# Kernel tuning notes

Measured on AMD Instinct MI355X. Metric: run time of the kernel, lower is better.

## Reference

```python
import jax, jax.numpy as jnp
import numpy as np

N = 20000          # nodes
E = 320000         # directed edges (self-loops added in reference)
F_IN = 128         # input node features
HEADS = 8
HID = 64           # per-head hidden channels
G = 64             # graphs in the batch
NUM_CLASSES = 10
NEG_SLOPE = 0.2    # PyG GATConv LeakyReLU slope


def _gat_layer(x, src, dst, W, a_src, a_dst, bias, n_nodes):
    """PyG-style GATConv: messages flow src->dst, softmax over incoming edges."""
    H, C = a_src.shape
    h = (x @ W).reshape(n_nodes, H, C)                     # [N,H,C]
    asrc = jnp.einsum('nhc,hc->nh', h, a_src)              # [N,H]
    adst = jnp.einsum('nhc,hc->nh', h, a_dst)              # [N,H]
    e = jax.nn.leaky_relu(asrc[src] + adst[dst], NEG_SLOPE)  # [Etot,H]
    emax = jax.ops.segment_max(e, dst, num_segments=n_nodes)  # [N,H]
    ee = jnp.exp(e - emax[dst])
    denom = jax.ops.segment_sum(ee, dst, num_segments=n_nodes)
    alpha = ee / (denom[dst] + 1e-16)                      # [Etot,H]
    out = jax.ops.segment_sum(h[src] * alpha[:, :, None], dst, num_segments=n_nodes)
    return out.reshape(n_nodes, H * C) + bias


def setup_inputs() -> dict:
    key = jax.random.key(0)
    ks = jax.random.split(key, 10)
    x = jax.random.normal(ks[0], (N, F_IN), jnp.float32)
    edge_index = jax.random.randint(ks[1], (2, E), 0, N, jnp.int32)
    batch = jnp.sort(jax.random.randint(ks[2], (N,), 0, G, jnp.int32))
    # layer 1: F_IN -> HEADS*HID (concat)
    W1 = jax.random.normal(ks[3], (F_IN, HEADS * HID), jnp.float32) / np.float32(np.sqrt(F_IN))
    a_src1 = jax.random.normal(ks[4], (HEADS, HID), jnp.float32) / np.float32(np.sqrt(HID))
    a_dst1 = jax.random.normal(ks[5], (HEADS, HID), jnp.float32) / np.float32(np.sqrt(HID))
    b1 = jnp.zeros((HEADS * HID,), jnp.float32)
    # layer 2: HEADS*HID -> NUM_CLASSES (1 head)
    W2 = jax.random.normal(ks[6], (HEADS * HID, NUM_CLASSES), jnp.float32) / np.float32(np.sqrt(HEADS * HID))
    a_src2 = jax.random.normal(ks[7], (1, NUM_CLASSES), jnp.float32) / np.float32(np.sqrt(NUM_CLASSES))
    a_dst2 = jax.random.normal(ks[8], (1, NUM_CLASSES), jnp.float32) / np.float32(np.sqrt(NUM_CLASSES))
    b2 = jnp.zeros((NUM_CLASSES,), jnp.float32)
    return {"x": x, "edge_index": edge_index, "batch": batch,
            "W1": W1, "a_src1": a_src1, "a_dst1": a_dst1, "b1": b1,
            "W2": W2, "a_src2": a_src2, "a_dst2": a_dst2, "b2": b2}


def reference(x, edge_index, batch, W1, a_src1, a_dst1, b1, W2, a_src2, a_dst2, b2):
    n = x.shape[0]
    loop = jnp.arange(n, dtype=edge_index.dtype)   # add_self_loops=True (PyG default)
    src = jnp.concatenate([edge_index[0], loop])
    dst = jnp.concatenate([edge_index[1], loop])
    h = jax.nn.elu(_gat_layer(x, src, dst, W1, a_src1, a_dst1, b1, n))
    h = _gat_layer(h, src, dst, W2, a_src2, a_dst2, b2, n)
    # PowerMeanAggregation with default p=1.0 == mean pooling per graph
    sums = jax.ops.segment_sum(h, batch, num_segments=G)                    # [G,NC]
    counts = jax.ops.segment_sum(jnp.ones((n, 1), h.dtype), batch, num_segments=G)
    return sums / jnp.maximum(counts, 1.0)
```

## Files before the change

### kernel.cpp

```cpp
#include <hip/hip_runtime.h>
#include <hip/hip_bf16.h>

typedef unsigned short ushort_t;
typedef unsigned int uint_t;
typedef unsigned char uchar_t;

typedef __attribute__((ext_vector_type(8))) short bf16x8;
typedef __attribute__((ext_vector_type(4))) float f32x4;
typedef __attribute__((ext_vector_type(2))) float f32x2;

__device__ __forceinline__ float bf2f(ushort_t u) {
    union { uint_t i; float f; } v; v.i = ((uint_t)u) << 16; return v.f;
}
__device__ __forceinline__ ushort_t f2bf(float f) {
    __hip_bfloat16 h = __float2bfloat16(f);
    ushort_t u; __builtin_memcpy(&u, &h, 2); return u;
}
__device__ __forceinline__ uchar_t f2fp8(float v) {
    int p = __builtin_amdgcn_cvt_pk_fp8_f32(v, v, 0, false);
    return (uchar_t)(p & 0xff);
}
__device__ __forceinline__ float leaky(float v) { return (v > 0.f) ? v : 0.2f * v; }

#define PO_AS1 0
#define PO_AD1 512
#define PO_B1  1024
#define PO_W2  1536
#define PO_AS2 6656
#define PO_AD2 6666
#define PO_B2  6676
#define PTOT   6686

__device__ __forceinline__ bool detect_fp32_local(const ushort_t* __restrict__ xa) {
    __shared__ int cnt;
    if (threadIdx.x == 0) cnt = 0;
    __syncthreads();
    int bad = 0;
    for (int i = threadIdx.x; i < 4096; i += 256) {
        float v = bf2f(xa[i]);
        if (!(fabsf(v) < 1e4f)) bad++;
    }
    if (bad) atomicAdd(&cnt, bad);
    __syncthreads();
    return cnt >= 16;
}

__global__ __launch_bounds__(256) void k_prep(const void* __restrict__ x,
                                              const void* __restrict__ W1,
                                              const void* as1, const void* ad1,
                                              const void* b1, const void* W2,
                                              const void* as2, const void* ad2,
                                              const void* b2,
                                              ushort_t* __restrict__ W1t,
                                              float* __restrict__ prm,
                                              int* __restrict__ deg,
                                              int* __restrict__ flag, int N) {
    int b = blockIdx.x, t = threadIdx.x;
    if (b < 283) {
        bool isf = detect_fp32_local((const ushort_t*)x);
        if (b == 0 && t == 0) *flag = isf ? 1 : 0;
        if (b < 256) {
            int idx = b * 256 + t;
            int n = idx & 511, k = idx >> 9;
            float v = isf ? ((const float*)W1)[k * 512 + n]
                          : bf2f(((const ushort_t*)W1)[k * 512 + n]);
            W1t[n * 128 + k] = f2bf(v);
        } else {
            int i = (b - 256) * 256 + t;
            if (i < PTOT) {
                const void* src; int off;
                if (i < 512)       { src = as1; off = i; }
                else if (i < 1024) { src = ad1; off = i - 512; }
                else if (i < 1536) { src = b1;  off = i - 1024; }
                else if (i < 6656) { src = W2;  off = i - 1536; }
                else if (i < 6666) { src = as2; off = i - 6656; }
                else if (i < 6676) { src = ad2; off = i - 6666; }
                else               { src = b2;  off = i - 6676; }
                prm[i] = isf ? ((const float*)src)[off] : bf2f(((const ushort_t*)src)[off]);
            }
        }
    } else {
        int i = (b - 283) * 256 + t;
        if (i < N) deg[i] = 0;
    }
}

__global__ __launch_bounds__(256) void k_gemm_hist(const void* __restrict__ xraw,
                                                   const ushort_t* __restrict__ w1t,
                                                   const float* __restrict__ prm,
                                                   const int* __restrict__ ei,
                                                   const int* __restrict__ flag,
                                                   uchar_t* __restrict__ h1,
                                                   float* __restrict__ asrcf,
                                                   float* __restrict__ adstf,
                                                   int* __restrict__ deg,
                                                   int E, int Etot) {
    int b = blockIdx.x, t = threadIdx.x;
    if (b >= 1250) {
        int e = (b - 1250) * 256 + t;
        if (e < Etot) {
            int dst = (e < E) ? ei[E + e] : (e - E);
            atomicAdd(&deg[dst], 1);
        }
        return;
    }
    int wave = t >> 6, lane = t & 63;
    int m0 = b * 16;
    bool isf = (*flag != 0);
    __shared__ ushort_t sA[16 * 128];
    {
        ushort_t tmp[8];
        if (isf) {
            const float4* x4 = (const float4*)((const float*)xraw + (size_t)m0 * 128);
            float4 f0 = x4[2 * t], f1 = x4[2 * t + 1];
            tmp[0] = f2bf(f0.x); tmp[1] = f2bf(f0.y); tmp[2] = f2bf(f0.z); tmp[3] = f2bf(f0.w);
            tmp[4] = f2bf(f1.x); tmp[5] = f2bf(f1.y); tmp[6] = f2bf(f1.z); tmp[7] = f2bf(f1.w);
        } else {
            const uint4* x4 = (const uint4*)((const ushort_t*)xraw + (size_t)m0 * 128);
            uint4 u = x4[t];
            __builtin_memcpy(tmp, &u, 16);
        }
        *reinterpret_cast<uint4*>(&sA[t * 8]) = *reinterpret_cast<uint4*>(tmp);
    }
    __syncthreads();
    int mr = lane & 15, quad = lane >> 4;
    int n0 = wave * 128;
    f32x4 acc[8];
#pragma unroll
    for (int ct = 0; ct < 8; ++ct) acc[ct] = {0.f, 0.f, 0.f, 0.f};
#pragma unroll
    for (int kk = 0; kk < 4; ++kk) {
        bf16x8 a = *reinterpret_cast<const bf16x8*>(&sA[mr * 128 + quad * 8 + kk * 32]);
#pragma unroll
        for (int ct = 0; ct < 8; ++ct) {
            bf16x8 bb = *reinterpret_cast<const bf16x8*>(
                &w1t[(size_t)(n0 + ct * 16 + mr) * 128 + quad * 8 + kk * 32]);
            acc[ct] = __builtin_amdgcn_mfma_f32_16x16x32_bf16(a, bb, acc[ct], 0, 0, 0);
        }
    }
    int col = lane & 15;
#pragma unroll
    for (int hh = 0; hh < 2; ++hh) {
        float ps[4] = {0.f, 0.f, 0.f, 0.f}, pd[4] = {0.f, 0.f, 0.f, 0.f};
#pragma unroll
        for (int c4 = 0; c4 < 4; ++c4) {
            int ct = hh * 4 + c4;
            int abscol = n0 + ct * 16 + col;
            float asv = prm[PO_AS1 + abscol];
            float adv = prm[PO_AD1 + abscol];
#pragma unroll
            for (int r = 0; r < 4; ++r) {
                h1[(size_t)(m0 + quad * 4 + r) * 512 + abscol] = f2fp8(acc[ct][r]);
                ps[r] += acc[ct][r] * asv;
                pd[r] += acc[ct][r] * adv;
            }
        }
#pragma unroll
        for (int off = 1; off <= 8; off <<= 1) {
#pragma unroll
            for (int r = 0; r < 4; ++r) {
                ps[r] += __shfl_xor(ps[r], off, 64);
                pd[r] += __shfl_xor(pd[r], off, 64);
            }
        }
        if (col == 0) {
            int head = 2 * wave + hh;
#pragma unroll
            for (int r = 0; r < 4; ++r) {
                asrcf[(m0 + quad * 4 + r) * 8 + head] = ps[r];
                adstf[(m0 + quad * 4 + r) * 8 + head] = pd[r];
            }
        }
    }
}

__global__ __launch_bounds__(256) void k_scan(const int* __restrict__ deg,
                                              int* __restrict__ rowptr,
                                              int* __restrict__ cursor, int N) {
    int b = blockIdx.x, t = threadIdx.x;
    int lane = t & 63, wv = t >> 6;
    __shared__ int ws[4], wt[4];
    __shared__ int sbase;
    int limit = b * 256;
    int partial = 0;
    for (int i = t; i < limit; i += 256) partial += deg[i];
#pragma unroll
    for (int off = 32; off; off >>= 1) partial += __shfl_xor(partial, off, 64);
    if (lane == 0) ws[wv] = partial;
    __syncthreads();
    if (t == 0) sbase = ws[0] + ws[1] + ws[2] + ws[3];
    __syncthreads();
    int base = sbase;
    int i = limit + t;
    int v = (i < N) ? deg[i] : 0;
    int inc = v;
#pragma unroll
    for (int off = 1; off < 64; off <<= 1) {
        int u = __shfl_up(inc, off, 64);
        if (lane >= off) inc += u;
    }
    if (lane == 63) wt[wv] = inc;
    __syncthreads();
    int woff = 0;
    for (int w = 0; w < 4; ++w) if (w < wv) woff += wt[w];
    int excl = base + woff + inc - v;
    if (i < N) { rowptr[i + 1] = excl + v; cursor[i] = excl; }
    if (i == 0) rowptr[0] = 0;
}

__global__ void k_scatter(const int* __restrict__ ei, int* __restrict__ cursor,
                          int* __restrict__ csr_src, int E, int Etot) {
    int e = blockIdx.x * 256 + threadIdx.x;
    if (e >= Etot) return;
    int src, dst;
    if (e < E) { src = ei[e]; dst = ei[E + e]; } else { src = dst = e - E; }
    int pos = atomicAdd(&cursor[dst], 1);
    csr_src[pos] = src;
}

__global__ __launch_bounds__(256) void k_agg1(const uchar_t* __restrict__ h1,
                                              const float* __restrict__ asrcf,
                                              const float* __restrict__ adstf,
                                              const int* __restrict__ rowptr,
                                              const int* __restrict__ csr_src,
                                              const float* __restrict__ prm,
                                              float* __restrict__ h2,
                                              float* __restrict__ asrc2f,
                                              float* __restrict__ adst2f) {
    int n = blockIdx.x * 4 + (threadIdx.x >> 6);
    int lane = threadIdx.x & 63;
    int hh = lane >> 3;
    int cb = lane * 8;
    int start = rowptr[n], end = rowptr[n + 1];
    int deg = end - start;
    float adh = adstf[n * 8 + hh];
    float a0 = 0.f, a1 = 0.f, a2 = 0.f, a3 = 0.f, a4 = 0.f, a5 = 0.f, a6 = 0.f, a7 = 0.f;
    float den = 0.f;
    for (int base = 0; base < deg; base += 64) {
        int m = min(64, deg - base);
        int sIdx = csr_src[start + base + min(lane, m - 1)];
        for (int g = 0; g < m; g += 8) {
            int s[8]; float lo[8]; uint2 p[8];
#pragma unroll
            for (int j = 0; j < 8; ++j)
                s[j] = __shfl(sIdx, min(g + j, m - 1), 64);
#pragma unroll
            for (int j = 0; j < 8; ++j)
                lo[j] = asrcf[s[j] * 8 + hh];
#pragma unroll
            for (int j = 0; j < 8; ++j)
                p[j] = *reinterpret_cast<const uint2*>(&h1[(size_t)s[j] * 512 + cb]);
#pragma unroll
            for (int j = 0; j < 8; ++j) {
                float we = (g + j < m) ? __expf(leaky(lo[j] + adh)) : 0.f;
                den += we;
                f32x2 q0 = __builtin_amdgcn_cvt_pk_f32_fp8((int)p[j].x, false);
                f32x2 q1 = __builtin_amdgcn_cvt_pk_f32_fp8((int)p[j].x, true);
                f32x2 q2 = __builtin_amdgcn_cvt_pk_f32_fp8((int)p[j].y, false);
                f32x2 q3 = __builtin_amdgcn_cvt_pk_f32_fp8((int)p[j].y, true);
                a0 += we * q0.x; a1 += we * q0.y;
                a2 += we * q1.x; a3 += we * q1.y;
                a4 += we * q2.x; a5 += we * q2.y;
                a6 += we * q3.x; a7 += we * q3.y;
            }
        }
    }
    float inv = 1.f / (den + 1e-16f);
    float r[8] = {a0, a1, a2, a3, a4, a5, a6, a7};
    float p2[10];
#pragma unroll
    for (int c = 0; c < 10; ++c) p2[c] = 0.f;
#pragma unroll
    for (int j = 0; j < 8; ++j) {
        float rv = r[j] * inv + prm[PO_B1 + cb + j];
        rv = (rv > 0.f) ? rv : expm1f(rv);
#pragma unroll
        for (int c = 0; c < 10; ++c)
            p2[c] += rv * prm[PO_W2 + (cb + j) * 10 + c];
    }
#pragma unroll
    for (int c = 0; c < 10; ++c)
#pragma unroll
        for (int off = 32; off; off >>= 1)
            p2[c] += __shfl_xor(p2[c], off, 64);
    if (lane == 0) {
        float as = 0.f, ad = 0.f;
#pragma unroll
        for (int c = 0; c < 10; ++c) {
            h2[n * 12 + c] = p2[c];
            as += p2[c] * prm[PO_AS2 + c];
            ad += p2[c] * prm[PO_AD2 + c];
        }
        asrc2f[n] = as; adst2f[n] = ad;
    }
}

__global__ __launch_bounds__(256) void k_agg2(const float* __restrict__ h2,
                                              const float* __restrict__ asrc2f,
                                              const float* __restrict__ adst2f,
                                              const int* __restrict__ rowptr,
                                              const int* __restrict__ csr_src,
                                              const float* __restrict__ prm,
                                              float* __restrict__ out2) {
    int n = blockIdx.x * 4 + (threadIdx.x >> 6);
    int l = threadIdx.x & 63;
    int start = rowptr[n], end = rowptr[n + 1];
    float adn = adst2f[n];
    float den = 0.f;
    float oc[10];
#pragma unroll
    for (int c = 0; c < 10; ++c) oc[c] = 0.f;
    int e = start + l;
    int s_cur = (e < end) ? csr_src[e] : 0;
    for (; e < end; ) {
        int e_next = e + 64;
        int s_next = (e_next < end) ? csr_src[e_next] : 0;
        float lo = asrc2f[s_cur];
        const float4* hp = reinterpret_cast<const float4*>(&h2[s_cur * 12]);
        float4 q0 = hp[0], q1 = hp[1], q2 = hp[2];
        float ee = __expf(leaky(lo + adn));
        den += ee;
        oc[0] += ee * q0.x; oc[1] += ee * q0.y; oc[2] += ee * q0.z; oc[3] += ee * q0.w;
        oc[4] += ee * q1.x; oc[5] += ee * q1.y; oc[6] += ee * q1.z; oc[7] += ee * q1.w;
        oc[8] += ee * q2.x; oc[9] += ee * q2.y;
        e = e_next; s_cur = s_next;
    }
#pragma unroll
    for (int off = 32; off; off >>= 1) {
        den += __shfl_xor(den, off, 64);
#pragma unroll
        for (int c = 0; c < 10; ++c) oc[c] += __shfl_xor(oc[c], off, 64);
    }
    if (l == 0) {
        float inv = 1.f / (den + 1e-16f);
        for (int c = 0; c < 10; ++c) out2[n * 10 + c] = oc[c] * inv + prm[PO_B2 + c];
    }
}

__global__ __launch_bounds__(256) void k_pool(const float* __restrict__ out2,
                                              const int* __restrict__ batch,
                                              const int* __restrict__ flag,
                                              void* __restrict__ dout, int N) {
    bool isf = (*flag != 0);
    int g = blockIdx.x, t = threadIdx.x;
    __shared__ int s_lo, s_hi;
    __shared__ float sm[256];
    if (t == 0) {
        int lo = 0, hi = N;
        while (lo < hi) { int mid = (lo + hi) >> 1; if (batch[mid] < g) lo = mid + 1; else hi = mid; }
        s_lo = lo;
        int lo2 = lo, hi2 = N;
        while (lo2 < hi2) { int mid = (lo2 + hi2) >> 1; if (batch[mid] < g + 1) lo2 = mid + 1; else hi2 = mid; }
        s_hi = lo2;
    }
    __syncthreads();
    int lo = s_lo, hi = s_hi;
    float acc[10];
#pragma unroll
    for (int c = 0; c < 10; ++c) acc[c] = 0.f;
    for (int i = lo + t; i < hi; i += 256)
#pragma unroll
        for (int c = 0; c < 10; ++c) acc[c] += out2[i * 10 + c];
    float cnt = (float)((hi - lo) > 0 ? (hi - lo) : 1);
    for (int c = 0; c < 10; ++c) {
        sm[t] = acc[c]; __syncthreads();
        for (int off = 128; off; off >>= 1) {
            if (t < off) sm[t] += sm[t + off];
            __syncthreads();
        }
        if (t == 0) {
            float r = sm[0] / cnt;
            if (isf) ((float*)dout)[g * 10 + c] = r;
            else     ((ushort_t*)dout)[g * 10 + c] = f2bf(r);
        }
        __syncthreads();
    }
}

extern "C" void kernel_launch(void* const* d_in, const int* in_sizes, int n_in,
                              void* d_out, int out_size, void* d_ws, size_t ws_size,
                              hipStream_t stream) {
    const void* x   = d_in[0];
    const int* ei   = (const int*)d_in[1];
    const int* batch= (const int*)d_in[2];
    const void* W1  = d_in[3];
    const void* as1 = d_in[4];
    const void* ad1 = d_in[5];
    const void* b1  = d_in[6];
    const void* W2  = d_in[7];
    const void* as2 = d_in[8];
    const void* ad2 = d_in[9];
    const void* b2  = d_in[10];

    constexpr int N = 20000, E = 320000, Etot = E + N;
    constexpr int histBlocks = (Etot + 255) / 256;

    char* p = (char*)d_ws;
    auto alloc = [&](size_t bytes) {
        char* r = p; p += (bytes + 255) & ~(size_t)255; return r;
    };
    int* flag       = (int*)alloc(256);
    float* prm      = (float*)alloc((size_t)PTOT * 4);
    ushort_t* w1t   = (ushort_t*)alloc(512 * 128 * 2);
    uchar_t* h1     = (uchar_t*)alloc((size_t)N * 512);
    float* asrc1f   = (float*)alloc((size_t)N * 8 * 4);
    float* adst1f   = (float*)alloc((size_t)N * 8 * 4);
    float* asrc2f   = (float*)alloc((size_t)N * 4);
    float* adst2f   = (float*)alloc((size_t)N * 4);
    float* h2       = (float*)alloc((size_t)N * 12 * 4);
    float* out2     = (float*)alloc((size_t)N * 10 * 4);
    int* deg        = (int*)alloc((size_t)N * 4);
    int* rowptr     = (int*)alloc((size_t)(N + 1) * 4);
    int* cursor     = (int*)alloc((size_t)N * 4);
    int* csr_src    = (int*)alloc((size_t)Etot * 4);

    k_prep<<<362, 256, 0, stream>>>(x, W1, as1, ad1, b1, W2, as2, ad2, b2,
                                    w1t, prm, deg, flag, N);
    k_gemm_hist<<<1250 + histBlocks, 256, 0, stream>>>(x, w1t, prm, ei, flag, h1,
                                                       asrc1f, adst1f, deg, E, Etot);
    k_scan<<<(N + 255) / 256, 256, 0, stream>>>(deg, rowptr, cursor, N);
    k_scatter<<<histBlocks, 256, 0, stream>>>(ei, cursor, csr_src, E, Etot);
    k_agg1<<<N / 4, 256, 0, stream>>>(h1, asrc1f, adst1f, rowptr, csr_src, prm,
                                      h2, asrc2f, adst2f);
    k_agg2<<<N / 4, 256, 0, stream>>>(h2, asrc2f, adst2f, rowptr, csr_src, prm, out2);
    k_pool<<<64, 256, 0, stream>>>(out2, batch, flag, d_out, N);
}
```

Before: 253.5 us.

## Precompute edge attention weights in scatter, split agg1 per node, fuse pooling into agg2

The scatter kernel now computes the per-edge, per-head exp(leaky) attention weights and stores them in CSR order, so agg1 reads them directly instead of gathering asrc and recomputing exp. Agg1 splits each node's edges across two wavefronts and combines the partial sums through shared memory. Agg2 uses 16 lanes per node and pads h2 to 16 floats. It also fuses mean pooling by accumulating per-graph sums with atomics, which replaces the separate pool kernel with a tiny final divide kernel. The cost is an extra weight write and read of Etot*8 floats, plus float atomics that make summation order nondeterministic.

```diff
diff --git a/kernel.cpp b/kernel.cpp
--- a/kernel.cpp
+++ b/kernel.cpp
@@ -54,6 +54,7 @@
                                               ushort_t* __restrict__ W1t,
                                               float* __restrict__ prm,
                                               int* __restrict__ deg,
+                                              float* __restrict__ gacc,
                                               int* __restrict__ flag, int N) {
     int b = blockIdx.x, t = threadIdx.x;
     if (b < 283) {
@@ -79,9 +80,11 @@
                 prm[i] = isf ? ((const float*)src)[off] : bf2f(((const ushort_t*)src)[off]);
             }
         }
-    } else {
+    } else if (b < 362) {
         int i = (b - 283) * 256 + t;
         if (i < N) deg[i] = 0;
+    } else {
+        for (int i = t; i < 640; i += 256) gacc[i] = 0.f;
     }
 }
 
@@ -208,51 +211,75 @@
     if (i == 0) rowptr[0] = 0;
 }
 
-__global__ void k_scatter(const int* __restrict__ ei, int* __restrict__ cursor,
-                          int* __restrict__ csr_src, int E, int Etot) {
+__global__ __launch_bounds__(256) void k_scatter(const int* __restrict__ ei,
+                                                 int* __restrict__ cursor,
+                                                 const float* __restrict__ asrcf,
+                                                 const float* __restrict__ adstf,
+                                                 int* __restrict__ csr_src,
+                                                 float* __restrict__ wcsr,
+                                                 int E, int Etot) {
     int e = blockIdx.x * 256 + threadIdx.x;
     if (e >= Etot) return;
     int src, dst;
     if (e < E) { src = ei[e]; dst = ei[E + e]; } else { src = dst = e - E; }
     int pos = atomicAdd(&cursor[dst], 1);
     csr_src[pos] = src;
+    const float4* ap = (const float4*)&asrcf[(size_t)src * 8];
+    const float4* bp = (const float4*)&adstf[(size_t)dst * 8];
+    float4 a0 = ap[0], a1 = ap[1];
+    float4 b0 = bp[0], b1 = bp[1];
+    float4 w0, w1;
+    w0.x = __expf(leaky(a0.x + b0.x));
+    w0.y = __expf(leaky(a0.y + b0.y));
+    w0.z = __expf(leaky(a0.z + b0.z));
+    w0.w = __expf(leaky(a0.w + b0.w));
+    w1.x = __expf(leaky(a1.x + b1.x));
+    w1.y = __expf(leaky(a1.y + b1.y));
+    w1.z = __expf(leaky(a1.z + b1.z));
+    w1.w = __expf(leaky(a1.w + b1.w));
+    float4* wp = (float4*)&wcsr[(size_t)pos * 8];
+    wp[0] = w0; wp[1] = w1;
 }
 
 __global__ __launch_bounds__(256) void k_agg1(const uchar_t* __restrict__ h1,
-                                              const float* __restrict__ asrcf,
-                                              const float* __restrict__ adstf,
                                               const int* __restrict__ rowptr,
                                               const int* __restrict__ csr_src,
+                                              const float* __restrict__ wcsr,
                                               const float* __restrict__ prm,
                                               float* __restrict__ h2,
                                               float* __restrict__ asrc2f,
                                               float* __restrict__ adst2f) {
-    int n = blockIdx.x * 4 + (threadIdx.x >> 6);
+    int wid = threadIdx.x >> 6;
+    int ni = wid >> 1;
+    int half = wid & 1;
+    int n = blockIdx.x * 2 + ni;
     int lane = threadIdx.x & 63;
     int hh = lane >> 3;
     int cb = lane * 8;
     int start = rowptr[n], end = rowptr[n + 1];
     int deg = end - start;
-    float adh = adstf[n * 8 + hh];
+    int mid = (deg + 1) >> 1;
+    int es = start + (half ? mid : 0);
+    int ee = half ? end : (start + mid);
     float a0 = 0.f, a1 = 0.f, a2 = 0.f, a3 = 0.f, a4 = 0.f, a5 = 0.f, a6 = 0.f, a7 = 0.f;
     float den = 0.f;
-    for (int base = 0; base < deg; base += 64) {
-        int m = min(64, deg - base);
-        int sIdx = csr_src[start + base + min(lane, m - 1)];
+    for (int base = es; base < ee; base += 64) {
+        int m = min(64, ee - base);
+        int sIdx = csr_src[base + min(lane, m - 1)];
         for (int g = 0; g < m; g += 8) {
-            int s[8]; float lo[8]; uint2 p[8];
+            int s[8]; float w[8]; uint2 p[8];
 #pragma unroll
             for (int j = 0; j < 8; ++j)
                 s[j] = __shfl(sIdx, min(g + j, m - 1), 64);
 #pragma unroll
             for (int j = 0; j < 8; ++j)
-                lo[j] = asrcf[s[j] * 8 + hh];
+                w[j] = wcsr[(size_t)(base + min(g + j, m - 1)) * 8 + hh];
 #pragma unroll
             for (int j = 0; j < 8; ++j)
                 p[j] = *reinterpret_cast<const uint2*>(&h1[(size_t)s[j] * 512 + cb]);
 #pragma unroll
             for (int j = 0; j < 8; ++j) {
-                float we = (g + j < m) ? __expf(leaky(lo[j] + adh)) : 0.f;
+                float we = (g + j < m) ? w[j] : 0.f;
                 den += we;
                 f32x2 q0 = __builtin_amdgcn_cvt_pk_f32_fp8((int)p[j].x, false);
                 f32x2 q1 = __builtin_amdgcn_cvt_pk_f32_fp8((int)p[j].x, true);
@@ -265,6 +292,19 @@
             }
         }
     }
+    __shared__ float sred[2][64][9];
+    if (half) {
+        float* sp = sred[ni][lane];
+        sp[0] = a0; sp[1] = a1; sp[2] = a2; sp[3] = a3;
+        sp[4] = a4; sp[5] = a5; sp[6] = a6; sp[7] = a7; sp[8] = den;
+    }
+    __syncthreads();
+    if (half) return;
+    {
+        const float* sp = sred[ni][lane];
+        a0 += sp[0]; a1 += sp[1]; a2 += sp[2]; a3 += sp[3];
+        a4 += sp[4]; a5 += sp[5]; a6 += sp[6]; a7 += sp[7]; den += sp[8];
+    }
     float inv = 1.f / (den + 1e-16f);
     float r[8] = {a0, a1, a2, a3, a4, a5, a6, a7};
     float p2[10];
@@ -287,7 +327,7 @@
         float as = 0.f, ad = 0.f;
 #pragma unroll
         for (int c = 0; c < 10; ++c) {
-            h2[n * 12 + c] = p2[c];
+            h2[(size_t)n * 16 + c] = p2[c];
             as += p2[c] * prm[PO_AS2 + c];
             ad += p2[c] * prm[PO_AD2 + c];
         }
@@ -301,79 +341,75 @@
                                               const int* __restrict__ rowptr,
                                               const int* __restrict__ csr_src,
                                               const float* __restrict__ prm,
-                                              float* __restrict__ out2) {
-    int n = blockIdx.x * 4 + (threadIdx.x >> 6);
-    int l = threadIdx.x & 63;
+                                              const int* __restrict__ batch,
+                                              float* __restrict__ gacc) {
+    int t = threadIdx.x;
+    int grp = t >> 4, l = t & 15;
+    int n = blockIdx.x * 16 + grp;
     int start = rowptr[n], end = rowptr[n + 1];
     float adn = adst2f[n];
     float den = 0.f;
     float oc[10];
 #pragma unroll
     for (int c = 0; c < 10; ++c) oc[c] = 0.f;
-    int e = start + l;
-    int s_cur = (e < end) ? csr_src[e] : 0;
-    for (; e < end; ) {
-        int e_next = e + 64;
-        int s_next = (e_next < end) ? csr_src[e_next] : 0;
-        float lo = asrc2f[s_cur];
-        const float4* hp = reinterpret_cast<const float4*>(&h2[s_cur * 12]);
-        float4 q0 = hp[0], q1 = hp[1], q2 = hp[2];
+    for (int e = start + l; e < end; e += 16) {
+        int s = csr_src[e];
+        float lo = asrc2f[s];
+        const float4* hp = reinterpret_cast<const float4*>(&h2[(size_t)s * 16]);
+        float4 q0 = hp[0], q1 = hp[1];
+        float2 q2 = *reinterpret_cast<const float2*>(&h2[(size_t)s * 16 + 8]);
         float ee = __expf(leaky(lo + adn));
         den += ee;
         oc[0] += ee * q0.x; oc[1] += ee * q0.y; oc[2] += ee * q0.z; oc[3] += ee * q0.w;
         oc[4] += ee * q1.x; oc[5] += ee * q1.y; oc[6] += ee * q1.z; oc[7] += ee * q1.w;
         oc[8] += ee * q2.x; oc[9] += ee * q2.y;
-        e = e_next; s_cur = s_next;
-    }
-#pragma unroll
-    for (int off = 32; off; off >>= 1) {
+    }
+#pragma unroll
+    for (int off = 8; off; off >>= 1) {
         den += __shfl_xor(den, off, 64);
 #pragma unroll
         for (int c = 0; c < 10; ++c) oc[c] += __shfl_xor(oc[c], off, 64);
     }
+    __shared__ float sres[16][11];
+    __shared__ int sg[16];
     if (l == 0) {
-        float inv = 1.f / (den + 1e-16f);
-        for (int c = 0; c < 10; ++c) out2[n * 10 + c] = oc[c] * inv + prm[PO_B2 + c];
-    }
-}
-
-__global__ __launch_bounds__(256) void k_pool(const float* __restrict__ out2,
-                                              const int* __restrict__ batch,
-                                              const int* __restrict__ flag,
-                                              void* __restrict__ dout, int N) {
+        float invd = 1.f / (den + 1e-16f);
+#pragma unroll
+        for (int c = 0; c < 10; ++c) sres[grp][c] = oc[c] * invd + prm[PO_B2 + c];
+        sg[grp] = batch[n];
+    }
+    __syncthreads();
+    if (t < 10) {
+        int c = t;
+        float run = sres[0][c]; int g = sg[0];
+        for (int k = 1; k < 16; ++k) {
+            if (sg[k] != g) {
+                atomicAdd(&gacc[g * 10 + c], run);
+                g = sg[k]; run = 0.f;
+            }
+            run += sres[k][c];
+        }
+        atomicAdd(&gacc[g * 10 + c], run);
+    }
+}
+
+__global__ void k_final(const float* __restrict__ gacc,
+                        const int* __restrict__ batch,
+                        const int* __restrict__ flag,
+                        void* __restrict__ dout, int N) {
+    int g = threadIdx.x;
+    if (g >= 64) return;
     bool isf = (*flag != 0);
-    int g = blockIdx.x, t = threadIdx.x;
-    __shared__ int s_lo, s_hi;
-    __shared__ float sm[256];
-    if (t == 0) {
-        int lo = 0, hi = N;
-        while (lo < hi) { int mid = (lo + hi) >> 1; if (batch[mid] < g) lo = mid + 1; else hi = mid; }
-        s_lo = lo;
-        int lo2 = lo, hi2 = N;
-        while (lo2 < hi2) { int mid = (lo2 + hi2) >> 1; if (batch[mid] < g + 1) lo2 = mid + 1; else hi2 = mid; }
-        s_hi = lo2;
-    }
-    __syncthreads();
-    int lo = s_lo, hi = s_hi;
-    float acc[10];
-#pragma unroll
-    for (int c = 0; c < 10; ++c) acc[c] = 0.f;
-    for (int i = lo + t; i < hi; i += 256)
-#pragma unroll
-        for (int c = 0; c < 10; ++c) acc[c] += out2[i * 10 + c];
-    float cnt = (float)((hi - lo) > 0 ? (hi - lo) : 1);
+    int lo = 0, hi = N;
+    while (lo < hi) { int mid = (lo + hi) >> 1; if (batch[mid] < g) lo = mid + 1; else hi = mid; }
+    int lo2 = lo, hi2 = N;
+    while (lo2 < hi2) { int mid = (lo2 + hi2) >> 1; if (batch[mid] < g + 1) lo2 = mid + 1; else hi2 = mid; }
+    int count = lo2 - lo;
+    float cnt = (float)(count > 0 ? count : 1);
     for (int c = 0; c < 10; ++c) {
-        sm[t] = acc[c]; __syncthreads();
-        for (int off = 128; off; off >>= 1) {
-            if (t < off) sm[t] += sm[t + off];
-            __syncthreads();
-        }
-        if (t == 0) {
-            float r = sm[0] / cnt;
-            if (isf) ((float*)dout)[g * 10 + c] = r;
-            else     ((ushort_t*)dout)[g * 10 + c] = f2bf(r);
-        }
-        __syncthreads();
+        float r = gacc[g * 10 + c] / cnt;
+        if (isf) ((float*)dout)[g * 10 + c] = r;
+        else     ((ushort_t*)dout)[g * 10 + c] = f2bf(r);
     }
 }
 
@@ -407,21 +443,24 @@
     float* adst1f   = (float*)alloc((size_t)N * 8 * 4);
     float* asrc2f   = (float*)alloc((size_t)N * 4);
     float* adst2f   = (float*)alloc((size_t)N * 4);
-    float* h2       = (float*)alloc((size_t)N * 12 * 4);
-    float* out2     = (float*)alloc((size_t)N * 10 * 4);
+    float* h2       = (float*)alloc((size_t)N * 16 * 4);
+    float* gacc     = (float*)alloc((size_t)64 * 10 * 4);
     int* deg        = (int*)alloc((size_t)N * 4);
     int* rowptr     = (int*)alloc((size_t)(N + 1) * 4);
     int* cursor     = (int*)alloc((size_t)N * 4);
     int* csr_src    = (int*)alloc((size_t)Etot * 4);
-
-    k_prep<<<362, 256, 0, stream>>>(x, W1, as1, ad1, b1, W2, as2, ad2, b2,
-                                    w1t, prm, deg, flag, N);
+    float* wcsr     = (float*)alloc((size_t)Etot * 8 * 4);
+
+    k_prep<<<363, 256, 0, stream>>>(x, W1, as1, ad1, b1, W2, as2, ad2, b2,
+                                    w1t, prm, deg, gacc, flag, N);
     k_gemm_hist<<<1250 + histBlocks, 256, 0, stream>>>(x, w1t, prm, ei, flag, h1,
                                                        asrc1f, adst1f, deg, E, Etot);
     k_scan<<<(N + 255) / 256, 256, 0, stream>>>(deg, rowptr, cursor, N);
-    k_scatter<<<histBlocks, 256, 0, stream>>>(ei, cursor, csr_src, E, Etot);
-    k_agg1<<<N / 4, 256, 0, stream>>>(h1, asrc1f, adst1f, rowptr, csr_src, prm,
+    k_scatter<<<histBlocks, 256, 0, stream>>>(ei, cursor, asrc1f, adst1f,
+                                              csr_src, wcsr, E, Etot);
+    k_agg1<<<N / 2, 256, 0, stream>>>(h1, rowptr, csr_src, wcsr, prm,
                                       h2, asrc2f, adst2f);
-    k_agg2<<<N / 4, 256, 0, stream>>>(h2, asrc2f, adst2f, rowptr, csr_src, prm, out2);
-    k_pool<<<64, 256, 0, stream>>>(out2, batch, flag, d_out, N);
-}
+    k_agg2<<<N / 16, 256, 0, stream>>>(h2, asrc2f, adst2f, rowptr, csr_src, prm,
+                                       batch, gacc);
+    k_final<<<1, 64, 0, stream>>>(gacc, batch, flag, d_out, N);
+}
```

Result: faster. 241.1 us (-4.9%).
